# Performance work log

Measured on AMD Instinct MI355X. Metric: run time of the kernel, lower is better.

The kernel has to match this reference:

```python
import jax, jax.numpy as jnp
import numpy as np

HIDDEN = 1024
NUM_EXPERTS = 8
TOP_K = 2
INNER = HIDDEN * 2
B, S = 4, 2048


def setup_inputs() -> dict:
    key = jax.random.key(0)
    ks = jax.random.split(key, 8)
    sd = 1.0 / np.sqrt(HIDDEN)
    si = 1.0 / np.sqrt(INNER)
    return {
        "x": jax.random.normal(ks[0], (B, S, HIDDEN), dtype=jnp.float32),
        "Wr": jax.random.uniform(ks[1], (HIDDEN, NUM_EXPERTS), jnp.float32, -sd, sd),
        "br": jax.random.uniform(ks[2], (NUM_EXPERTS,), jnp.float32, -sd, sd),
        "W1": jax.random.uniform(ks[3], (NUM_EXPERTS, HIDDEN, INNER), jnp.float32, -sd, sd),
        "b1": jax.random.uniform(ks[4], (NUM_EXPERTS, INNER), jnp.float32, -sd, sd),
        "W2": jax.random.uniform(ks[5], (NUM_EXPERTS, INNER, HIDDEN), jnp.float32, -si, si),
        "b2": jax.random.uniform(ks[6], (NUM_EXPERTS, HIDDEN), jnp.float32, -si, si),
    }


def reference(x, Wr, br, W1, b1, W2, b2):
    batch, seq, hidden = x.shape
    tokens = x.reshape(-1, hidden)                       # [N, d]
    n = tokens.shape[0]
    logits = tokens @ Wr + br                            # [N, E]
    top_w, top_i = jax.lax.top_k(logits, TOP_K)          # [N, k]
    top_w = jax.nn.softmax(top_w, axis=-1)
    # Dense per-token expert weights (zero outside top-k) — equivalent to the
    # sorted-dispatch + index_add combine in the original.
    weights = jnp.zeros((n, NUM_EXPERTS), dtype=top_w.dtype)
    weights = weights.at[jnp.arange(n)[:, None], top_i].add(top_w)  # [N, E]
    out = jnp.zeros_like(tokens)
    for e in range(NUM_EXPERTS):  # fixed small loop over experts
        h = jax.nn.relu(tokens @ W1[e] + b1[e])          # [N, inner]
        y = h @ W2[e] + b2[e]                            # [N, d]
        out = out + y * weights[:, e:e + 1]
    return out.reshape(batch, seq, hidden)
```

## Files before the change

kernel.cpp:

```cpp
#include <hip/hip_runtime.h>
#include <stdint.h>

#define HID    1024
#define EXPERTS 8
#define TOPK   2
#define INNER  2048
#define NTOK   8192
#define NPAIR  (NTOK * TOPK)
#define MAXT   136

#define BM 128
#define BN 128
#define BK 64

typedef _Float16 f16;
typedef f16   f16x8 __attribute__((ext_vector_type(8)));
typedef float f32x4 __attribute__((ext_vector_type(4)));

__device__ __forceinline__ void gload_lds16(const void* g, void* l) {
  __builtin_amdgcn_global_load_lds(
      (const __attribute__((address_space(1))) void*)g,
      (__attribute__((address_space(3))) void*)l, 16, 0, 0);
}

__global__ void router_kernel(const float* __restrict__ x,
                              const float* __restrict__ Wr,
                              const float* __restrict__ br,
                              int* __restrict__ e_sel, float* __restrict__ w_sel) {
  int gid  = blockIdx.x * blockDim.x + threadIdx.x;
  int wid  = gid >> 6;
  int lane = gid & 63;
  if (wid >= NTOK) return;

  const f32x4* xr = (const f32x4*)(x + (size_t)wid * HID);
  float acc[EXPERTS];
#pragma unroll
  for (int e = 0; e < EXPERTS; ++e) acc[e] = 0.f;

#pragma unroll
  for (int j = 0; j < HID / 256; ++j) {
    f32x4 xv = xr[j * 64 + lane];
    int   k  = (j * 64 + lane) * 4;
    const float* wr = Wr + (size_t)k * EXPERTS;
#pragma unroll
    for (int r = 0; r < 4; ++r) {
      float xs = xv[r];
      f32x4 w0 = *(const f32x4*)(wr + r * 8);
      f32x4 w1 = *(const f32x4*)(wr + r * 8 + 4);
#pragma unroll
      for (int e = 0; e < 4; ++e) { acc[e] += xs * w0[e]; acc[4 + e] += xs * w1[e]; }
    }
  }
#pragma unroll
  for (int e = 0; e < EXPERTS; ++e) {
#pragma unroll
    for (int off = 32; off > 0; off >>= 1) acc[e] += __shfl_xor(acc[e], off);
  }
  if (lane == 0) {
    float lg[EXPERTS];
#pragma unroll
    for (int e = 0; e < EXPERTS; ++e) lg[e] = acc[e] + br[e];
    int e0 = 0; float l0 = lg[0];
#pragma unroll
    for (int e = 1; e < EXPERTS; ++e) if (lg[e] > l0) { l0 = lg[e]; e0 = e; }
    int e1 = -1; float l1 = -3.4e38f;
#pragma unroll
    for (int e = 0; e < EXPERTS; ++e) if (e != e0 && lg[e] > l1) { l1 = lg[e]; e1 = e; }
    float a  = __expf(l1 - l0);
    float w0 = 1.f / (1.f + a);
    float w1 = a * w0;
    e_sel[wid * 2]     = e0;  e_sel[wid * 2 + 1] = e1;
    w_sel[wid * 2]     = w0;  w_sel[wid * 2 + 1] = w1;
  }
}

__global__ __launch_bounds__(1024) void dispatch_kernel(
    const int* __restrict__ e_sel, const float* __restrict__ w_sel,
    int* __restrict__ tok_list, float* __restrict__ wt_list,
    int* __restrict__ counts, int* __restrict__ bases,
    int* __restrict__ tile_e, int* __restrict__ tile_m0,
    int* __restrict__ tinfo) {
  __shared__ int scnt[EXPERTS][1024];
  __shared__ int etot[EXPERTS];
  __shared__ int ebase[EXPERTS];
  int tid = threadIdx.x, lane = tid & 63, wv = tid >> 6;

  int myE[16]; float myW[16];
  int lc[EXPERTS];
#pragma unroll
  for (int e = 0; e < EXPERTS; ++e) lc[e] = 0;
#pragma unroll
  for (int i = 0; i < 16; ++i) {
    int p = tid * 16 + i;
    myE[i] = e_sel[p];
    myW[i] = w_sel[p];
#pragma unroll
    for (int e = 0; e < EXPERTS; ++e) lc[e] += (myE[i] == e);
  }
#pragma unroll
  for (int e = 0; e < EXPERTS; ++e) scnt[e][tid] = lc[e];
  __syncthreads();

  if (wv < EXPERTS) {
    int run = 0;
    for (int c = 0; c < 16; ++c) {
      int v = scnt[wv][c * 64 + lane];
      int incl = v;
#pragma unroll
      for (int off = 1; off < 64; off <<= 1) {
        int n = __shfl_up(incl, off);
        if (lane >= off) incl += n;
      }
      scnt[wv][c * 64 + lane] = run + incl - v;
      run += __shfl(incl, 63);
    }
    if (lane == 0) etot[wv] = run;
  }
  __syncthreads();

  if (tid == 0) {
    int s = 0, t = 0;
    for (int e = 0; e < EXPERTS; ++e) {
      ebase[e] = s; bases[e] = s; counts[e] = etot[e];
      for (int m0 = 0; m0 < etot[e]; m0 += BM) { tile_e[t] = e; tile_m0[t] = m0; ++t; }
      s += etot[e];
    }
    tinfo[0] = t;
  }
  __syncthreads();

  int cur[EXPERTS];
#pragma unroll
  for (int e = 0; e < EXPERTS; ++e) cur[e] = ebase[e] + scnt[e][tid];
#pragma unroll
  for (int i = 0; i < 16; ++i) {
    int p = 0;
#pragma unroll
    for (int e = 0; e < EXPERTS; ++e) if (myE[i] == e) p = cur[e]++;
    tok_list[p] = (tid * 16 + i) >> 1;
    wt_list[p]  = myW[i];
  }
}

__global__ void convert_x_kernel(const float* __restrict__ x,
                                 f16* __restrict__ x16, int n8) {
  int i = blockIdx.x * blockDim.x + threadIdx.x;
  int stride = gridDim.x * blockDim.x;
  for (; i < n8; i += stride) {
    f32x4 a = ((const f32x4*)x)[i * 2];
    f32x4 b = ((const f32x4*)x)[i * 2 + 1];
    f16x8 o;
#pragma unroll
    for (int j = 0; j < 4; ++j) { o[j] = (f16)a[j]; o[4 + j] = (f16)b[j]; }
    ((f16x8*)x16)[i] = o;
  }
}

__global__ void transpose_cvt_kernel(const float* __restrict__ src,
                                     f16* __restrict__ dst, int R, int C) {
  __shared__ float tile[32][33];
  int z = blockIdx.z;
  src += (size_t)z * R * C;
  dst += (size_t)z * R * C;
  int c0 = blockIdx.x * 32, r0 = blockIdx.y * 32;
  int tx = threadIdx.x, ty = threadIdx.y;
#pragma unroll
  for (int i = 0; i < 4; ++i)
    tile[ty + i * 8][tx] = src[(size_t)(r0 + ty + i * 8) * C + c0 + tx];
  __syncthreads();
#pragma unroll
  for (int i = 0; i < 4; ++i)
    dst[(size_t)(c0 + ty + i * 8) * R + r0 + tx] = (f16)tile[tx][ty + i * 8];
}


#define GEMM_STAGE(AS, BS) do {                                   \
  _Pragma("unroll") for (int i_ = 0; i_ < 4; ++i_) {              \
    gload_lds16(gA[i_], &(AS)[i_ * 2048 + wid * 512]);            \
    gload_lds16(gB[i_], &(BS)[i_ * 2048 + wid * 512]);            \
    gA[i_] += BK; gB[i_] += BK;                                   \
  }                                                               \
} while (0)

#define GEMM_COMPUTE(AS, BS) do {                                               \
  _Pragma("unroll") for (int kk_ = 0; kk_ < 2; ++kk_) {                         \
    int cko_ = kk_ ? colk1 : colk0;                                             \
    f16x8 af_[4], bf_[4];                                                       \
    _Pragma("unroll") for (int mi_ = 0; mi_ < 4; ++mi_)                         \
      af_[mi_] = *(const f16x8*)&(AS)[(wm + mi_ * 16 + ar) * 64 + cko_];        \
    _Pragma("unroll") for (int ni_ = 0; ni_ < 4; ++ni_)                         \
      bf_[ni_] = *(const f16x8*)&(BS)[(wn + ni_ * 16 + ar) * 64 + cko_];        \
    _Pragma("unroll") for (int mi_ = 0; mi_ < 4; ++mi_)                         \
      _Pragma("unroll") for (int ni_ = 0; ni_ < 4; ++ni_)                       \
        acc[mi_][ni_] = __builtin_amdgcn_mfma_f32_16x16x32_f16(                 \
            af_[mi_], bf_[ni_], acc[mi_][ni_], 0, 0, 0);                        \
  }                                                                             \
} while (0)

__global__ __launch_bounds__(256) void gemm1_kernel(
    const f16* __restrict__ x16, const f16* __restrict__ w1t,
    const float* __restrict__ b1, const int* __restrict__ tok_list,
    const int* __restrict__ counts, const int* __restrict__ bases,
    const int* __restrict__ tile_e, const int* __restrict__ tile_m0,
    const int* __restrict__ tinfo, int c0,
    f16* __restrict__ h16) {
  int g = blockIdx.y;
  int t = c0 + g;
  if (t >= tinfo[0]) return;
  int e    = tile_e[t];
  int m0   = tile_m0[t];
  int cnt  = counts[e];
  int base = bases[e];
  int n0   = blockIdx.x * BN;
  const f16* Bg = w1t + (size_t)e * INNER * HID;

  __shared__ f16 As0[BM * BK], As1[BM * BK];
  __shared__ f16 Bs0[BM * BK], Bs1[BM * BK];

  int tid = threadIdx.x;
  int lane = tid & 63, wid = tid >> 6;
  int wm = (wid >> 1) * 64, wn = (wid & 1) * 64;

  int trow = tid >> 3;
  int gcol = (tid & 7) ^ (trow & 7);
  const f16* gA[4];
  const f16* gB[4];
#pragma unroll
  for (int i = 0; i < 4; ++i) {
    int row = i * 32 + trow;
    int tok = tok_list[base + min(m0 + row, cnt - 1)];
    gA[i] = x16 + (size_t)tok * HID + gcol * 8;
    gB[i] = Bg + (size_t)(n0 + row) * HID + gcol * 8;
  }

  f32x4 acc[4][4];
#pragma unroll
  for (int i = 0; i < 4; ++i)
#pragma unroll
    for (int j = 0; j < 4; ++j) acc[i][j] = (f32x4){0.f, 0.f, 0.f, 0.f};

  int ar = lane & 15, hi = lane >> 4;
  int sa = ar & 7;
  int colk0 = ((hi) ^ sa) * 8;
  int colk1 = ((4 + hi) ^ sa) * 8;

  GEMM_STAGE(As0, Bs0);
  __syncthreads();
  for (int ks = 0; ks < HID / BK; ks += 2) {
    GEMM_STAGE(As1, Bs1);
    GEMM_COMPUTE(As0, Bs0);
    __syncthreads();
    if (ks + 2 < HID / BK) GEMM_STAGE(As0, Bs0);
    GEMM_COMPUTE(As1, Bs1);
    __syncthreads();
  }

  int col = lane & 15, rb = hi * 4;
  float bb[4];
#pragma unroll
  for (int ni = 0; ni < 4; ++ni) bb[ni] = b1[e * INNER + n0 + wn + ni * 16 + col];
#pragma unroll
  for (int mi = 0; mi < 4; ++mi)
#pragma unroll
    for (int r = 0; r < 4; ++r) {
      int ml = wm + mi * 16 + rb + r;
      if (m0 + ml < cnt) {
        size_t rowoff = (size_t)(g * BM + ml) * INNER + n0 + wn + col;
#pragma unroll
        for (int ni = 0; ni < 4; ++ni) {
          float v = acc[mi][ni][r] + bb[ni];
          h16[rowoff + ni * 16] = (f16)fmaxf(v, 0.f);
        }
      }
    }
}

__global__ __launch_bounds__(256) void gemm2_kernel(
    const f16* __restrict__ h16, const f16* __restrict__ w2t,
    const float* __restrict__ b2, const int* __restrict__ tok_list,
    const float* __restrict__ wt_list, const int* __restrict__ counts,
    const int* __restrict__ bases,
    const int* __restrict__ tile_e, const int* __restrict__ tile_m0,
    const int* __restrict__ tinfo, int c0,
    float* __restrict__ out) {
  int g = blockIdx.y;
  int t = c0 + g;
  if (t >= tinfo[0]) return;
  int e    = tile_e[t];
  int m0   = tile_m0[t];
  int cnt  = counts[e];
  int base = bases[e];
  int d0   = blockIdx.x * BN;
  const f16* Bg = w2t + (size_t)e * HID * INNER;

  __shared__ f16 As0[BM * BK], As1[BM * BK];
  __shared__ f16 Bs0[BM * BK], Bs1[BM * BK];

  int tid = threadIdx.x;
  int lane = tid & 63, wid = tid >> 6;
  int wm = (wid >> 1) * 64, wn = (wid & 1) * 64;

  int trow = tid >> 3;
  int gcol = (tid & 7) ^ (trow & 7);
  const f16* gA[4];
  const f16* gB[4];
#pragma unroll
  for (int i = 0; i < 4; ++i) {
    int row  = i * 32 + trow;
    int lrow = min(m0 + row, cnt - 1) - m0;
    gA[i] = h16 + (size_t)(g * BM + lrow) * INNER + gcol * 8;
    gB[i] = Bg + (size_t)(d0 + row) * INNER + gcol * 8;
  }

  f32x4 acc[4][4];
#pragma unroll
  for (int i = 0; i < 4; ++i)
#pragma unroll
    for (int j = 0; j < 4; ++j) acc[i][j] = (f32x4){0.f, 0.f, 0.f, 0.f};

  int ar = lane & 15, hi = lane >> 4;
  int sa = ar & 7;
  int colk0 = ((hi) ^ sa) * 8;
  int colk1 = ((4 + hi) ^ sa) * 8;

  GEMM_STAGE(As0, Bs0);
  __syncthreads();
  for (int ks = 0; ks < INNER / BK; ks += 2) {
    GEMM_STAGE(As1, Bs1);
    GEMM_COMPUTE(As0, Bs0);
    __syncthreads();
    if (ks + 2 < INNER / BK) GEMM_STAGE(As0, Bs0);
    GEMM_COMPUTE(As1, Bs1);
    __syncthreads();
  }

  int col = lane & 15, rb = hi * 4;
  float bb[4];
#pragma unroll
  for (int ni = 0; ni < 4; ++ni) bb[ni] = b2[e * HID + d0 + wn + ni * 16 + col];
#pragma unroll
  for (int mi = 0; mi < 4; ++mi)
#pragma unroll
    for (int r = 0; r < 4; ++r) {
      int ml = wm + mi * 16 + rb + r;
      if (m0 + ml < cnt) {
        int   p   = base + m0 + ml;
        int   tok = tok_list[p];
        float w   = wt_list[p];
        float* orow = out + (size_t)tok * HID + d0 + wn + col;
#pragma unroll
        for (int ni = 0; ni < 4; ++ni) {
          float v = acc[mi][ni][r] + bb[ni];
          atomicAdd(orow + ni * 16, v * w);
        }
      }
    }
}

extern "C" void kernel_launch(void* const* d_in, const int* in_sizes, int n_in,
                              void* d_out, int out_size, void* d_ws, size_t ws_size,
                              hipStream_t stream) {
  (void)in_sizes; (void)n_in;
  const float* x  = (const float*)d_in[0];
  const float* Wr = (const float*)d_in[1];
  const float* br = (const float*)d_in[2];
  const float* W1 = (const float*)d_in[3];
  const float* b1 = (const float*)d_in[4];
  const float* W2 = (const float*)d_in[5];
  const float* b2 = (const float*)d_in[6];
  float* out = (float*)d_out;

  char*  ws  = (char*)d_ws;
  size_t off = 0;
  auto alloc = [&](size_t bytes) {
    char* p = ws + off;
    off += bytes; off = (off + 255) & ~(size_t)255;
    return p;
  };
  int*   tok_list = (int*)alloc(NPAIR * sizeof(int));
  float* wt_list  = (float*)alloc(NPAIR * sizeof(float));
  int*   e_sel    = (int*)alloc(NTOK * 2 * sizeof(int));
  float* w_sel    = (float*)alloc(NTOK * 2 * sizeof(float));
  int*   counts   = (int*)alloc(EXPERTS * sizeof(int));
  int*   bases    = (int*)alloc(EXPERTS * sizeof(int));
  int*   tile_e   = (int*)alloc(MAXT * sizeof(int));
  int*   tile_m0  = (int*)alloc(MAXT * sizeof(int));
  int*   tinfo    = (int*)alloc(16 * sizeof(int));
  f16*   w1t      = (f16*)alloc((size_t)EXPERTS * HID * INNER * sizeof(f16));
  f16*   w2t      = (f16*)alloc((size_t)EXPERTS * HID * INNER * sizeof(f16));
  f16*   x16      = (f16*)alloc((size_t)NTOK * HID * sizeof(f16));
  const size_t TILE_BYTES = (size_t)BM * INNER * sizeof(f16);
  size_t rem = (ws_size > off) ? (ws_size - off) : 0;
  int G = (int)(rem / TILE_BYTES);
  if (G < 1) G = 1;
  if (G > MAXT) G = MAXT;
  int nch = (MAXT + G - 1) / G;
  f16* h16 = (f16*)(ws + off);

  hipMemsetAsync(out, 0, (size_t)out_size * sizeof(float), stream);

  convert_x_kernel<<<2048, 256, 0, stream>>>(x, x16, NTOK * HID / 8);
  transpose_cvt_kernel<<<dim3(INNER / 32, HID / 32, EXPERTS), dim3(32, 8), 0, stream>>>(
      W1, w1t, HID, INNER);
  transpose_cvt_kernel<<<dim3(HID / 32, INNER / 32, EXPERTS), dim3(32, 8), 0, stream>>>(
      W2, w2t, INNER, HID);
  router_kernel<<<NTOK / 4, 256, 0, stream>>>(x, Wr, br, e_sel, w_sel);
  dispatch_kernel<<<1, 1024, 0, stream>>>(e_sel, w_sel, tok_list, wt_list,
                                          counts, bases, tile_e, tile_m0, tinfo);

  for (int c = 0; c < nch; ++c) {
    int c0 = c * G;
    int gy = (MAXT - c0 < G) ? (MAXT - c0) : G;
    gemm1_kernel<<<dim3(INNER / BN, gy, 1), 256, 0, stream>>>(
        x16, w1t, b1, tok_list, counts, bases, tile_e, tile_m0, tinfo, c0, h16);
    gemm2_kernel<<<dim3(HID / BN, gy, 1), 256, 0, stream>>>(
        h16, w2t, b2, tok_list, wt_list, counts, bases, tile_e, tile_m0, tinfo, c0, out);
  }
}
```

Before: 520.9 us.

## Widen GEMM tiles, triple-buffer LDS, split-K gemm2, expert-affine slot scheduling

Both expert GEMMs move from 128x128 tiles with 256 threads and double buffering to 128x256 tiles with 512 threads and a three-stage LDS pipeline that waits with explicit vmcnt. Tiles are mapped to slots interleaved by expert, so consecutive blocks on nearby CUs tend to share expert weights. gemm2 is split in K across two z-blocks that both atomically add into the output, with the bias applied only by the first. This aims to raise MFMA utilisation, hide load latency and spread gemm2 over more blocks, at the cost of more atomics, more LDS per block and many early-exit blocks on empty slots.

```diff
diff --git a/kernel.cpp b/kernel.cpp
--- a/kernel.cpp
+++ b/kernel.cpp
@@ -8,14 +8,18 @@
 #define NTOK   8192
 #define NPAIR  (NTOK * TOPK)
 #define MAXT   136
-
 #define BM 128
-#define BN 128
+#define BN 256
 #define BK 64
+#define NSLOT 304
+#define AFFS  24
 
 typedef _Float16 f16;
 typedef f16   f16x8 __attribute__((ext_vector_type(8)));
 typedef float f32x4 __attribute__((ext_vector_type(4)));
+
+#define VMCNT(n) asm volatile("s_waitcnt vmcnt(" #n ")" ::: "memory")
+#define BARRIER() do { __builtin_amdgcn_s_barrier(); asm volatile("" ::: "memory"); } while (0)
 
 __device__ __forceinline__ void gload_lds16(const void* g, void* l) {
   __builtin_amdgcn_global_load_lds(
@@ -36,7 +40,6 @@
   float acc[EXPERTS];
 #pragma unroll
   for (int e = 0; e < EXPERTS; ++e) acc[e] = 0.f;
-
 #pragma unroll
   for (int j = 0; j < HID / 256; ++j) {
     f32x4 xv = xr[j * 64 + lane];
@@ -78,8 +81,8 @@
     const int* __restrict__ e_sel, const float* __restrict__ w_sel,
     int* __restrict__ tok_list, float* __restrict__ wt_list,
     int* __restrict__ counts, int* __restrict__ bases,
-    int* __restrict__ tile_e, int* __restrict__ tile_m0,
-    int* __restrict__ tinfo) {
+    int* __restrict__ slot_e, int* __restrict__ slot_m0,
+    int* __restrict__ slot_g, int* __restrict__ tinfo) {
   __shared__ int scnt[EXPERTS][1024];
   __shared__ int etot[EXPERTS];
   __shared__ int ebase[EXPERTS];
@@ -118,14 +121,22 @@
   }
   __syncthreads();
 
+  if (tid < NSLOT) slot_e[tid] = -1;
+  __syncthreads();
   if (tid == 0) {
-    int s = 0, t = 0;
+    int s = 0;
     for (int e = 0; e < EXPERTS; ++e) {
-      ebase[e] = s; bases[e] = s; counts[e] = etot[e];
-      for (int m0 = 0; m0 < etot[e]; m0 += BM) { tile_e[t] = e; tile_m0[t] = m0; ++t; }
-      s += etot[e];
-    }
-    tinfo[0] = t;
+      ebase[e] = s; bases[e] = s; counts[e] = etot[e]; s += etot[e];
+    }
+    int ov = AFFS * EXPERTS, gt = 0;
+    for (int e = 0; e < EXPERTS; ++e) {
+      int ntl = (etot[e] + BM - 1) / BM;
+      for (int i = 0; i < ntl; ++i) {
+        int sl = (i < AFFS) ? (e + EXPERTS * i) : (ov++);
+        slot_e[sl] = e; slot_m0[sl] = i * BM; slot_g[sl] = gt++;
+      }
+    }
+    tinfo[0] = gt;
   }
   __syncthreads();
 
@@ -174,62 +185,80 @@
 }
 
 
-#define GEMM_STAGE(AS, BS) do {                                   \
-  _Pragma("unroll") for (int i_ = 0; i_ < 4; ++i_) {              \
-    gload_lds16(gA[i_], &(AS)[i_ * 2048 + wid * 512]);            \
-    gload_lds16(gB[i_], &(BS)[i_ * 2048 + wid * 512]);            \
-    gA[i_] += BK; gB[i_] += BK;                                   \
-  }                                                               \
+#define STAGE6(BUF) do {                                                      \
+  _Pragma("unroll") for (int i_ = 0; i_ < 2; ++i_) {                          \
+    gload_lds16(gA[i_], (BUF) + i_ * 4096 + wid * 512); gA[i_] += BK;         \
+  }                                                                           \
+  _Pragma("unroll") for (int i_ = 0; i_ < 4; ++i_) {                          \
+    gload_lds16(gB[i_], (BUF) + 8192 + i_ * 4096 + wid * 512); gB[i_] += BK;  \
+  }                                                                           \
 } while (0)
 
-#define GEMM_COMPUTE(AS, BS) do {                                               \
-  _Pragma("unroll") for (int kk_ = 0; kk_ < 2; ++kk_) {                         \
-    int cko_ = kk_ ? colk1 : colk0;                                             \
-    f16x8 af_[4], bf_[4];                                                       \
-    _Pragma("unroll") for (int mi_ = 0; mi_ < 4; ++mi_)                         \
-      af_[mi_] = *(const f16x8*)&(AS)[(wm + mi_ * 16 + ar) * 64 + cko_];        \
-    _Pragma("unroll") for (int ni_ = 0; ni_ < 4; ++ni_)                         \
-      bf_[ni_] = *(const f16x8*)&(BS)[(wn + ni_ * 16 + ar) * 64 + cko_];        \
-    _Pragma("unroll") for (int mi_ = 0; mi_ < 4; ++mi_)                         \
-      _Pragma("unroll") for (int ni_ = 0; ni_ < 4; ++ni_)                       \
-        acc[mi_][ni_] = __builtin_amdgcn_mfma_f32_16x16x32_f16(                 \
-            af_[mi_], bf_[ni_], acc[mi_][ni_], 0, 0, 0);                        \
-  }                                                                             \
+#define COMPUTE16(BUF) do {                                                   \
+  _Pragma("unroll") for (int kk_ = 0; kk_ < 2; ++kk_) {                       \
+    int lc_ = (kk_ * 4 + hi) ^ sa;                                            \
+    f16x8 af_[4], bf_[4];                                                     \
+    _Pragma("unroll") for (int mi_ = 0; mi_ < 4; ++mi_)                       \
+      af_[mi_] = *(const f16x8*)((BUF) + (wm + mi_ * 16 + ar) * 64 + lc_ * 8);\
+    _Pragma("unroll") for (int ni_ = 0; ni_ < 4; ++ni_)                       \
+      bf_[ni_] = *(const f16x8*)((BUF) + 8192 +                               \
+                                 (wn + ni_ * 16 + ar) * 64 + lc_ * 8);        \
+    _Pragma("unroll") for (int mi_ = 0; mi_ < 4; ++mi_)                       \
+      _Pragma("unroll") for (int ni_ = 0; ni_ < 4; ++ni_)                     \
+        acc[mi_][ni_] = __builtin_amdgcn_mfma_f32_16x16x32_f16(               \
+            af_[mi_], bf_[ni_], acc[mi_][ni_], 0, 0, 0);                      \
+  }                                                                           \
 } while (0)
 
-__global__ __launch_bounds__(256) void gemm1_kernel(
+#define PIPELINE_LOOP(NT) do {                                                \
+  STAGE6(q0); STAGE6(q1);                                                     \
+  VMCNT(6); BARRIER();                                                        \
+  for (int t = 0; t < (NT); ++t) {                                            \
+    if (t + 2 < (NT)) { STAGE6(q2); }                                         \
+    COMPUTE16(q0);                                                            \
+    if (t + 2 < (NT)) { VMCNT(6); } else { VMCNT(0); }                        \
+    BARRIER();                                                                \
+    f16* tm_ = q0; q0 = q1; q1 = q2; q2 = tm_;                                \
+  }                                                                           \
+} while (0)
+
+__global__ __launch_bounds__(512, 2) void gemm1_kernel(
     const f16* __restrict__ x16, const f16* __restrict__ w1t,
-    const float* __restrict__ b1, const int* __restrict__ tok_list,
+    const float* __restrict__ bias1, const int* __restrict__ tok_list,
     const int* __restrict__ counts, const int* __restrict__ bases,
-    const int* __restrict__ tile_e, const int* __restrict__ tile_m0,
-    const int* __restrict__ tinfo, int c0,
+    const int* __restrict__ slot_e, const int* __restrict__ slot_m0,
+    const int* __restrict__ slot_g, int c0, int G,
     f16* __restrict__ h16) {
-  int g = blockIdx.y;
-  int t = c0 + g;
-  if (t >= tinfo[0]) return;
-  int e    = tile_e[t];
-  int m0   = tile_m0[t];
-  int cnt  = counts[e];
-  int base = bases[e];
-  int n0   = blockIdx.x * BN;
+  int sx = blockIdx.x;
+  int e  = slot_e[sx];
+  if (e < 0) return;
+  int g  = slot_g[sx];
+  if (g < c0 || g >= c0 + G) return;
+  int m0 = slot_m0[sx];
+  int cnt = counts[e], base = bases[e];
+  int n0 = blockIdx.y * BN;
   const f16* Bg = w1t + (size_t)e * INNER * HID;
 
-  __shared__ f16 As0[BM * BK], As1[BM * BK];
-  __shared__ f16 Bs0[BM * BK], Bs1[BM * BK];
-
-  int tid = threadIdx.x;
-  int lane = tid & 63, wid = tid >> 6;
-  int wm = (wid >> 1) * 64, wn = (wid & 1) * 64;
+  __shared__ __align__(16) f16 LDS[3 * 24576];
+  f16 *q0 = LDS, *q1 = LDS + 24576, *q2 = LDS + 2 * 24576;
+
+  int tid = threadIdx.x, lane = tid & 63, wid = tid >> 6;
+  int wm = (wid >> 2) * 64, wn = (wid & 3) * 64;
+  int ar = lane & 15, hi = lane >> 4, sa = ar & 7;
 
   int trow = tid >> 3;
   int gcol = (tid & 7) ^ (trow & 7);
-  const f16* gA[4];
+  const f16* gA[2];
   const f16* gB[4];
 #pragma unroll
-  for (int i = 0; i < 4; ++i) {
-    int row = i * 32 + trow;
+  for (int i = 0; i < 2; ++i) {
+    int row = i * 64 + trow;
     int tok = tok_list[base + min(m0 + row, cnt - 1)];
     gA[i] = x16 + (size_t)tok * HID + gcol * 8;
+  }
+#pragma unroll
+  for (int i = 0; i < 4; ++i) {
+    int row = i * 64 + trow;
     gB[i] = Bg + (size_t)(n0 + row) * HID + gcol * 8;
   }
 
@@ -239,33 +268,20 @@
 #pragma unroll
     for (int j = 0; j < 4; ++j) acc[i][j] = (f32x4){0.f, 0.f, 0.f, 0.f};
 
-  int ar = lane & 15, hi = lane >> 4;
-  int sa = ar & 7;
-  int colk0 = ((hi) ^ sa) * 8;
-  int colk1 = ((4 + hi) ^ sa) * 8;
-
-  GEMM_STAGE(As0, Bs0);
-  __syncthreads();
-  for (int ks = 0; ks < HID / BK; ks += 2) {
-    GEMM_STAGE(As1, Bs1);
-    GEMM_COMPUTE(As0, Bs0);
-    __syncthreads();
-    if (ks + 2 < HID / BK) GEMM_STAGE(As0, Bs0);
-    GEMM_COMPUTE(As1, Bs1);
-    __syncthreads();
-  }
-
-  int col = lane & 15, rb = hi * 4;
+  PIPELINE_LOOP(HID / BK);
+
+  int colc = ar, rbase = hi * 4;
   float bb[4];
 #pragma unroll
-  for (int ni = 0; ni < 4; ++ni) bb[ni] = b1[e * INNER + n0 + wn + ni * 16 + col];
+  for (int ni = 0; ni < 4; ++ni)
+    bb[ni] = bias1[(size_t)e * INNER + n0 + wn + ni * 16 + colc];
 #pragma unroll
   for (int mi = 0; mi < 4; ++mi)
 #pragma unroll
     for (int r = 0; r < 4; ++r) {
-      int ml = wm + mi * 16 + rb + r;
+      int ml = wm + mi * 16 + rbase + r;
       if (m0 + ml < cnt) {
-        size_t rowoff = (size_t)(g * BM + ml) * INNER + n0 + wn + col;
+        size_t rowoff = (size_t)((g - c0) * BM + ml) * INNER + n0 + wn + colc;
 #pragma unroll
         for (int ni = 0; ni < 4; ++ni) {
           float v = acc[mi][ni][r] + bb[ni];
@@ -275,41 +291,47 @@
     }
 }
 
-__global__ __launch_bounds__(256) void gemm2_kernel(
+__global__ __launch_bounds__(512, 2) void gemm2_kernel(
     const f16* __restrict__ h16, const f16* __restrict__ w2t,
-    const float* __restrict__ b2, const int* __restrict__ tok_list,
+    const float* __restrict__ bias2, const int* __restrict__ tok_list,
     const float* __restrict__ wt_list, const int* __restrict__ counts,
     const int* __restrict__ bases,
-    const int* __restrict__ tile_e, const int* __restrict__ tile_m0,
-    const int* __restrict__ tinfo, int c0,
+    const int* __restrict__ slot_e, const int* __restrict__ slot_m0,
+    const int* __restrict__ slot_g, int c0, int G,
     float* __restrict__ out) {
-  int g = blockIdx.y;
-  int t = c0 + g;
-  if (t >= tinfo[0]) return;
-  int e    = tile_e[t];
-  int m0   = tile_m0[t];
-  int cnt  = counts[e];
-  int base = bases[e];
-  int d0   = blockIdx.x * BN;
+  int sx = blockIdx.x;
+  int e  = slot_e[sx];
+  if (e < 0) return;
+  int g  = slot_g[sx];
+  if (g < c0 || g >= c0 + G) return;
+  int m0 = slot_m0[sx];
+  int cnt = counts[e], base = bases[e];
+  int d0 = blockIdx.y * BN;
+  int kc = blockIdx.z;
+  int koff = kc * (INNER / 2);
   const f16* Bg = w2t + (size_t)e * HID * INNER;
 
-  __shared__ f16 As0[BM * BK], As1[BM * BK];
-  __shared__ f16 Bs0[BM * BK], Bs1[BM * BK];
-
-  int tid = threadIdx.x;
-  int lane = tid & 63, wid = tid >> 6;
-  int wm = (wid >> 1) * 64, wn = (wid & 1) * 64;
+  __shared__ __align__(16) f16 LDS[3 * 24576];
+  f16 *q0 = LDS, *q1 = LDS + 24576, *q2 = LDS + 2 * 24576;
+
+  int tid = threadIdx.x, lane = tid & 63, wid = tid >> 6;
+  int wm = (wid >> 2) * 64, wn = (wid & 3) * 64;
+  int ar = lane & 15, hi = lane >> 4, sa = ar & 7;
 
   int trow = tid >> 3;
   int gcol = (tid & 7) ^ (trow & 7);
-  const f16* gA[4];
+  const f16* gA[2];
   const f16* gB[4];
 #pragma unroll
+  for (int i = 0; i < 2; ++i) {
+    int row  = i * 64 + trow;
+    int lrow = min(m0 + row, cnt - 1) - m0;
+    gA[i] = h16 + ((size_t)(g - c0) * BM + lrow) * INNER + koff + gcol * 8;
+  }
+#pragma unroll
   for (int i = 0; i < 4; ++i) {
-    int row  = i * 32 + trow;
-    int lrow = min(m0 + row, cnt - 1) - m0;
-    gA[i] = h16 + (size_t)(g * BM + lrow) * INNER + gcol * 8;
-    gB[i] = Bg + (size_t)(d0 + row) * INNER + gcol * 8;
+    int row = i * 64 + trow;
+    gB[i] = Bg + (size_t)(d0 + row) * INNER + koff + gcol * 8;
   }
 
   f32x4 acc[4][4];
@@ -318,36 +340,23 @@
 #pragma unroll
     for (int j = 0; j < 4; ++j) acc[i][j] = (f32x4){0.f, 0.f, 0.f, 0.f};
 
-  int ar = lane & 15, hi = lane >> 4;
-  int sa = ar & 7;
-  int colk0 = ((hi) ^ sa) * 8;
-  int colk1 = ((4 + hi) ^ sa) * 8;
-
-  GEMM_STAGE(As0, Bs0);
-  __syncthreads();
-  for (int ks = 0; ks < INNER / BK; ks += 2) {
-    GEMM_STAGE(As1, Bs1);
-    GEMM_COMPUTE(As0, Bs0);
-    __syncthreads();
-    if (ks + 2 < INNER / BK) GEMM_STAGE(As0, Bs0);
-    GEMM_COMPUTE(As1, Bs1);
-    __syncthreads();
-  }
-
-  int col = lane & 15, rb = hi * 4;
+  PIPELINE_LOOP((INNER / 2) / BK);
+
+  int colc = ar, rbase = hi * 4;
   float bb[4];
 #pragma unroll
-  for (int ni = 0; ni < 4; ++ni) bb[ni] = b2[e * HID + d0 + wn + ni * 16 + col];
+  for (int ni = 0; ni < 4; ++ni)
+    bb[ni] = (kc == 0) ? bias2[(size_t)e * HID + d0 + wn + ni * 16 + colc] : 0.f;
 #pragma unroll
   for (int mi = 0; mi < 4; ++mi)
 #pragma unroll
     for (int r = 0; r < 4; ++r) {
-      int ml = wm + mi * 16 + rb + r;
+      int ml = wm + mi * 16 + rbase + r;
       if (m0 + ml < cnt) {
         int   p   = base + m0 + ml;
         int   tok = tok_list[p];
         float w   = wt_list[p];
-        float* orow = out + (size_t)tok * HID + d0 + wn + col;
+        float* orow = out + (size_t)tok * HID + d0 + wn + colc;
 #pragma unroll
         for (int ni = 0; ni < 4; ++ni) {
           float v = acc[mi][ni][r] + bb[ni];
@@ -383,8 +392,9 @@
   float* w_sel    = (float*)alloc(NTOK * 2 * sizeof(float));
   int*   counts   = (int*)alloc(EXPERTS * sizeof(int));
   int*   bases    = (int*)alloc(EXPERTS * sizeof(int));
-  int*   tile_e   = (int*)alloc(MAXT * sizeof(int));
-  int*   tile_m0  = (int*)alloc(MAXT * sizeof(int));
+  int*   slot_e   = (int*)alloc(NSLOT * sizeof(int));
+  int*   slot_m0  = (int*)alloc(NSLOT * sizeof(int));
+  int*   slot_g   = (int*)alloc(NSLOT * sizeof(int));
   int*   tinfo    = (int*)alloc(16 * sizeof(int));
   f16*   w1t      = (f16*)alloc((size_t)EXPERTS * HID * INNER * sizeof(f16));
   f16*   w2t      = (f16*)alloc((size_t)EXPERTS * HID * INNER * sizeof(f16));
@@ -406,14 +416,13 @@
       W2, w2t, INNER, HID);
   router_kernel<<<NTOK / 4, 256, 0, stream>>>(x, Wr, br, e_sel, w_sel);
   dispatch_kernel<<<1, 1024, 0, stream>>>(e_sel, w_sel, tok_list, wt_list,
-                                          counts, bases, tile_e, tile_m0, tinfo);
+                                          counts, bases, slot_e, slot_m0, slot_g, tinfo);
 
   for (int c = 0; c < nch; ++c) {
     int c0 = c * G;
-    int gy = (MAXT - c0 < G) ? (MAXT - c0) : G;
-    gemm1_kernel<<<dim3(INNER / BN, gy, 1), 256, 0, stream>>>(
-        x16, w1t, b1, tok_list, counts, bases, tile_e, tile_m0, tinfo, c0, h16);
-    gemm2_kernel<<<dim3(HID / BN, gy, 1), 256, 0, stream>>>(
-        h16, w2t, b2, tok_list, wt_list, counts, bases, tile_e, tile_m0, tinfo, c0, out);
-  }
-}
+    gemm1_kernel<<<dim3(NSLOT, INNER / BN, 1), 512, 0, stream>>>(
+        x16, w1t, b1, tok_list, counts, bases, slot_e, slot_m0, slot_g, c0, G, h16);
+    gemm2_kernel<<<dim3(NSLOT, HID / BN, 2), 512, 0, stream>>>(
+        h16, w2t, b2, tok_list, wt_list, counts, bases, slot_e, slot_m0, slot_g, c0, G, out);
+  }
+}
```

Result: slower. 533.4 us (+2.4%).
